# Kernel tuning notes

Hardware: AMD Instinct MI355X
Metric: run time of the kernel (lower is better)

The kernel has to match this reference:

```python
import jax, jax.numpy as jnp
import numpy as np

N, R, B, OUT, STD = 512, 4, 65536, 512, 0.01


def setup_inputs() -> dict:
    key = jax.random.key(0)
    ks = jax.random.split(key, 6)
    return {
        "x": jax.random.normal(ks[0], (B, N), jnp.float32),
        "G": jax.random.normal(ks[1], (N, R), jnp.float32) * STD,
        "H": jax.random.normal(ks[2], (N, R), jnp.float32) * STD,
        "b1": jax.random.normal(ks[3], (N,), jnp.float32) * STD,
        "W2": jax.random.normal(ks[4], (N, OUT), jnp.float32) * STD,
        "b2": jax.random.normal(ks[5], (OUT,), jnp.float32) * STD,
    }


def _shift_A(v):
    # Z_1 v: circular shift down with corner +1 (Toeplitz-like operator A)
    return jnp.concatenate([v[-1:], v[:-1]], axis=0)


def _shift_BT(v):
    # Z_{-1}^T v: shift up with corner -1 (Toeplitz-like operator B^T)
    return jnp.concatenate([v[1:], -v[:1]], axis=0)


def _krylov(shift_fn, V):
    # K[j, :, i] = A^j v_i, shape (n, n, r)
    def step(v, _):
        return shift_fn(v), v
    _, K = jax.lax.scan(step, V, None, length=V.shape[0])
    return K


def krylov_recon(G, H):
    # W = sum_i Krylov(Z_1, g_i) @ Krylov(Z_{-1}^T, h_i)^T, shape (n, n)
    KA = _krylov(_shift_A, G)   # (n, n, r)
    KB = _krylov(_shift_BT, H)  # (n, n, r)
    return jnp.einsum('jai,jbi->ab', KA, KB)


def reference(x, G, H, b1, W2, b2):
    W = krylov_recon(G, H)                 # (n, n) structured matrix
    h = jax.nn.relu(x @ W + b1)            # (B, n)
    return h @ W2 + b2                     # (B, out)
```

## Files before the change

kernel.cpp:

```cpp
#include <hip/hip_runtime.h>
#include <hip/hip_bf16.h>
#include <stdint.h>


typedef __attribute__((ext_vector_type(8))) short bf16x8;
typedef __attribute__((ext_vector_type(4))) float f32x4;
typedef __attribute__((ext_vector_type(4))) unsigned int u32x4;

__device__ __forceinline__ unsigned short f2bf(float f) {
  return __builtin_bit_cast(unsigned short, __float2bfloat16(f));
}

__global__ void build_w_partials(const float* __restrict__ G, const float* __restrict__ H,
                                 float* __restrict__ Wp) {
  __shared__ float4 Gs[512];
  __shared__ float4 Hs[512];
  const int t = threadIdx.x;
  const float4* G4 = (const float4*)G;
  const float4* H4 = (const float4*)H;
  for (int i = t; i < 512; i += 256) { Gs[i] = G4[i]; Hs[i] = H4[i]; }
  __syncthreads();

  const int blk  = blockIdx.x;
  const int tile = blk >> 2;
  const int jc   = blk & 3;
  const int a0 = (tile >> 3) << 6;
  const int b0 = (tile & 7) << 6;
  const int ab = a0 + ((t >> 4) << 2);
  const int bb = b0 + ((t & 15) << 2);

  float acc[4][4] = {};
  const int j0 = jc << 7;
  for (int jj = 0; jj < 128; ++jj) {
    const int j = j0 + jj;
    float4 Ga[4], Hb[4];
#pragma unroll
    for (int r = 0; r < 4; ++r) Ga[r] = Gs[(ab + r - j) & 511];
#pragma unroll
    for (int c = 0; c < 4; ++c) {
      const int idx = bb + c + j;
      const float s = (idx >= 512) ? -1.f : 1.f;
      const float4 hv = Hs[idx & 511];
      Hb[c].x = hv.x * s; Hb[c].y = hv.y * s; Hb[c].z = hv.z * s; Hb[c].w = hv.w * s;
    }
#pragma unroll
    for (int r = 0; r < 4; ++r)
#pragma unroll
      for (int c = 0; c < 4; ++c)
        acc[r][c] += Ga[r].x * Hb[c].x + Ga[r].y * Hb[c].y +
                     Ga[r].z * Hb[c].z + Ga[r].w * Hb[c].w;
  }

  float* outp = Wp + (size_t)jc * 262144;
#pragma unroll
  for (int r = 0; r < 4; ++r)
#pragma unroll
    for (int c = 0; c < 4; ++c)
      outp[(size_t)(ab + r) * 512 + (bb + c)] = acc[r][c];
}

__global__ void reduce_transpose_w(const float* __restrict__ Wp, unsigned short* __restrict__ Wt) {
  const int idx = blockIdx.x * 256 + threadIdx.x;
  const int b = idx >> 9, a = idx & 511;
  const size_t o = (size_t)a * 512 + b;
  float s = Wp[o] + Wp[o + 262144] + Wp[o + 524288] + Wp[o + 786432];
  Wt[(size_t)b * 512 + a] = f2bf(s);
}

__global__ void transpose_convert_w2(const float* __restrict__ W2, unsigned short* __restrict__ W2t) {
  const int idx = blockIdx.x * 256 + threadIdx.x;
  const int n = idx >> 9, k = idx & 511;
  W2t[(size_t)n * 512 + k] = f2bf(W2[(size_t)k * 512 + n]);
}

template <bool AF32>
__global__ __launch_bounds__(512, 2) void gemm_ring(
    const void* __restrict__ Ap, const unsigned short* __restrict__ Bt,
    const float* __restrict__ bias, void* __restrict__ Cp) {
  constexpr int NT    = 16;
  constexpr int RING  = AF32 ? 3 : 4;
  constexpr int ASLOT = AF32 ? 32768 : 16384;
  constexpr int BSLOT = 16384;
  constexpr int SLOT  = ASLOT + BSLOT;
  constexpr int NAG   = AF32 ? 4 : 2;
  constexpr int GPT   = NAG + 2;

  __shared__ __attribute__((aligned(16))) char lds[RING * SLOT];

  const int tid  = threadIdx.x;
  const int lane = tid & 63;
  const int w    = tid >> 6;
  const int wm   = w & 1;
  const int wn   = w >> 1;
  const int lr   = lane & 15;
  const int lq   = lane >> 4;

  const int bid = (int)blockIdx.x;
  const int wg  = (bid & 7) * 64 + (bid >> 3);
  const int m0  = (wg >> 1) << 8;
  const int n0  = (wg & 1) << 8;

  float bv[4];
#pragma unroll
  for (int ni = 0; ni < 4; ++ni) bv[ni] = bias[n0 + wn * 64 + ni * 16 + lr];
  asm volatile("s_waitcnt vmcnt(0) lgkmcnt(0)" ::: "memory");

  size_t aSrcOff[NAG];
  if constexpr (AF32) {
#pragma unroll
    for (int i = 0; i < 4; ++i) {
      const int cl = i * 512 + tid;
      const int r = cl >> 3, d = cl & 7;
      aSrcOff[i] = (size_t)r * 2048 + (size_t)((d ^ (r & 7)) << 4);
    }
  } else {
#pragma unroll
    for (int i = 0; i < 2; ++i) {
      const int cl = i * 512 + tid;
      const int r = cl >> 2, d = cl & 3;
      aSrcOff[i] = (size_t)r * 1024 + (size_t)((d ^ ((r >> 1) & 3)) << 4);
    }
  }
  size_t bSrcOff[2];
#pragma unroll
  for (int i = 0; i < 2; ++i) {
    const int cl = i * 512 + tid;
    const int r = cl >> 2, d = cl & 3;
    bSrcOff[i] = (size_t)r * 1024 + (size_t)((d ^ ((r >> 1) & 3)) << 4);
  }
  const char* aBase = (const char*)Ap + (size_t)m0 * (AF32 ? 2048 : 1024);
  const char* bBase = (const char*)Bt + (size_t)n0 * 1024;

  auto stage = [&](int kt) {
    char* sb = lds + (kt % RING) * SLOT;
#pragma unroll
    for (int i = 0; i < NAG; ++i)
      __builtin_amdgcn_global_load_lds(
        (const __attribute__((address_space(1))) void*)
          (aBase + aSrcOff[i] + (size_t)kt * (AF32 ? 128 : 64)),
        (__attribute__((address_space(3))) void*)(sb + i * 8192 + w * 1024),
        16, 0, 0);
#pragma unroll
    for (int i = 0; i < 2; ++i)
      __builtin_amdgcn_global_load_lds(
        (const __attribute__((address_space(1))) void*)
          (bBase + bSrcOff[i] + (size_t)kt * 64),
        (__attribute__((address_space(3))) void*)(sb + ASLOT + i * 8192 + w * 1024),
        16, 0, 0);
  };

  int offA[8], offB[4];
#pragma unroll
  for (int mi = 0; mi < 8; ++mi) {
    const int r = wm * 128 + mi * 16 + lr;
    if constexpr (AF32)
      offA[mi] = r * 128 + (((2 * lq) ^ (r & 7)) << 4);
    else
      offA[mi] = r * 64 + ((lq ^ ((r >> 1) & 3)) << 4);
  }
#pragma unroll
  for (int ni = 0; ni < 4; ++ni) {
    const int rb = wn * 64 + ni * 16 + lr;
    offB[ni] = ASLOT + rb * 64 + ((lq ^ ((rb >> 1) & 3)) << 4);
  }

  f32x4 acc[8][4];
  const f32x4 vz = {0.f, 0.f, 0.f, 0.f};
#pragma unroll
  for (int i = 0; i < 8; ++i)
#pragma unroll
    for (int j = 0; j < 4; ++j) acc[i][j] = vz;

#pragma unroll
  for (int p = 0; p < RING - 1; ++p) stage(p);
  if constexpr (AF32) asm volatile("s_waitcnt vmcnt(6)" ::: "memory");
  else                asm volatile("s_waitcnt vmcnt(8)" ::: "memory");
  __builtin_amdgcn_s_barrier();
  __builtin_amdgcn_sched_barrier(0);

#pragma unroll
  for (int t = 0; t < NT; ++t) {
    if (t + RING - 1 < NT) stage(t + RING - 1);

    const char* sb = lds + (t % RING) * SLOT;

    bf16x8 bfr[4];
#pragma unroll
    for (int ni = 0; ni < 4; ++ni) bfr[ni] = *(const bf16x8*)(sb + offB[ni]);

    if constexpr (AF32) {
      f32x4 lo[2][2], hi[2][2];
      bf16x8 afr[2];
#pragma unroll
      for (int p = 0; p < 2; ++p) {
        lo[0][p] = *(const f32x4*)(sb + offA[p]);
        hi[0][p] = *(const f32x4*)(sb + (offA[p] ^ 16));
      }
#pragma unroll
      for (int g = 0; g < 4; ++g) {
        if (g < 3) {
#pragma unroll
          for (int p = 0; p < 2; ++p) {
            lo[(g + 1) & 1][p] = *(const f32x4*)(sb + offA[2 * (g + 1) + p]);
            hi[(g + 1) & 1][p] = *(const f32x4*)(sb + (offA[2 * (g + 1) + p] ^ 16));
          }
        }
#pragma unroll
        for (int p = 0; p < 2; ++p) {
          const f32x4 l = lo[g & 1][p], h2 = hi[g & 1][p];
          unsigned int w0, w1, w2, w3;
          asm("v_cvt_pk_bf16_f32 %0, %1, %2" : "=v"(w0) : "v"(l.x), "v"(l.y));
          asm("v_cvt_pk_bf16_f32 %0, %1, %2" : "=v"(w1) : "v"(l.z), "v"(l.w));
          asm("v_cvt_pk_bf16_f32 %0, %1, %2" : "=v"(w2) : "v"(h2.x), "v"(h2.y));
          asm("v_cvt_pk_bf16_f32 %0, %1, %2" : "=v"(w3) : "v"(h2.z), "v"(h2.w));
          u32x4 pw = {w0, w1, w2, w3};
          afr[p] = __builtin_bit_cast(bf16x8, pw);
        }
        __builtin_amdgcn_s_setprio(1);
#pragma unroll
        for (int p = 0; p < 2; ++p)
#pragma unroll
          for (int ni = 0; ni < 4; ++ni)
            acc[2 * g + p][ni] =
                __builtin_amdgcn_mfma_f32_16x16x32_bf16(afr[p], bfr[ni], acc[2 * g + p][ni], 0, 0, 0);
        __builtin_amdgcn_s_setprio(0);
      }
    } else {
      bf16x8 afr[8];
#pragma unroll
      for (int p = 0; p < 2; ++p) afr[p] = *(const bf16x8*)(sb + offA[p]);
#pragma unroll
      for (int g = 0; g < 4; ++g) {
        if (g < 3) {
#pragma unroll
          for (int p = 0; p < 2; ++p)
            afr[2 * (g + 1) + p] = *(const bf16x8*)(sb + offA[2 * (g + 1) + p]);
        }
        __builtin_amdgcn_s_setprio(1);
#pragma unroll
        for (int p = 0; p < 2; ++p)
#pragma unroll
          for (int ni = 0; ni < 4; ++ni)
            acc[2 * g + p][ni] =
                __builtin_amdgcn_mfma_f32_16x16x32_bf16(afr[2 * g + p], bfr[ni], acc[2 * g + p][ni], 0, 0, 0);
        __builtin_amdgcn_s_setprio(0);
      }
    }

    if (t < NT - 1) {
      const int rem  = NT - 2 - t;
      const int keep = (rem < RING - 2 ? rem : RING - 2) * GPT;
      if (keep == 8)      asm volatile("s_waitcnt vmcnt(8)" ::: "memory");
      else if (keep == 6) asm volatile("s_waitcnt vmcnt(6)" ::: "memory");
      else if (keep == 4) asm volatile("s_waitcnt vmcnt(4)" ::: "memory");
      else                asm volatile("s_waitcnt vmcnt(0)" ::: "memory");
    }
    __builtin_amdgcn_s_barrier();
    __builtin_amdgcn_sched_barrier(0);
  }

#pragma unroll
  for (int ni = 0; ni < 4; ++ni) {
    const int gc = n0 + wn * 64 + ni * 16 + lr;
#pragma unroll
    for (int mi = 0; mi < 8; ++mi) {
      const int gr = m0 + wm * 128 + mi * 16 + lq * 4;
      const f32x4 v = acc[mi][ni];
#pragma unroll
      for (int i = 0; i < 4; ++i) {
        const float val = v[i] + bv[ni];
        if constexpr (AF32)
          ((unsigned short*)Cp)[(size_t)(gr + i) * 512 + gc] = f2bf(val > 0.f ? val : 0.f);
        else
          ((float*)Cp)[(size_t)(gr + i) * 512 + gc] = val;
      }
    }
  }
}

extern "C" void kernel_launch(void* const* d_in, const int* in_sizes, int n_in,
                              void* d_out, int out_size, void* d_ws, size_t ws_size,
                              hipStream_t stream) {
  (void)in_sizes; (void)n_in; (void)out_size; (void)ws_size;
  const float* x  = (const float*)d_in[0];
  const float* G  = (const float*)d_in[1];
  const float* H  = (const float*)d_in[2];
  const float* b1 = (const float*)d_in[3];
  const float* W2 = (const float*)d_in[4];
  const float* b2 = (const float*)d_in[5];
  float* out = (float*)d_out;

  char* ws = (char*)d_ws;
  unsigned short* h   = (unsigned short*)ws;
  unsigned short* Wt  = (unsigned short*)(ws + 67108864);
  unsigned short* W2t = (unsigned short*)(ws + 67633152);
  float*          Wp  = (float*)(ws + 68157440);

  build_w_partials<<<256, 256, 0, stream>>>(G, H, Wp);
  reduce_transpose_w<<<1024, 256, 0, stream>>>(Wp, Wt);
  transpose_convert_w2<<<1024, 256, 0, stream>>>(W2, W2t);
  gemm_ring<true><<<512, 512, 0, stream>>>((const void*)x, Wt, b1, (void*)h);
  gemm_ring<false><<<512, 512, 0, stream>>>((const void*)h, W2t, b2, (void*)out);
}
```

Baseline: 171.9 us.

## Shrink GEMM tiles to 128x128 with double-buffered LDS and more workgroups

Replaces the 256x256-tile, 512-thread GEMM that used a 3-4 deep async LDS ring with a 128x128-tile, 256-thread kernel using plain double buffering and __syncthreads. It launches 2048 workgroups instead of 512, targets 3 workgroups per CU, and drops the s_setprio and fine-grained vmcnt waits. The aim is higher occupancy and better load balance across CUs. The cost is lower arithmetic intensity per tile, so each operand is re-read from global memory more often, and less prefetch depth is available to hide latency.

```diff
diff --git a/kernel.cpp b/kernel.cpp
--- a/kernel.cpp
+++ b/kernel.cpp
@@ -74,18 +74,16 @@
 }
 
 template <bool AF32>
-__global__ __launch_bounds__(512, 2) void gemm_ring(
+__global__ __launch_bounds__(256, 3) void gemm_m97(
     const void* __restrict__ Ap, const unsigned short* __restrict__ Bt,
     const float* __restrict__ bias, void* __restrict__ Cp) {
   constexpr int NT    = 16;
-  constexpr int RING  = AF32 ? 3 : 4;
-  constexpr int ASLOT = AF32 ? 32768 : 16384;
-  constexpr int BSLOT = 16384;
-  constexpr int SLOT  = ASLOT + BSLOT;
+  constexpr int ASLOT = AF32 ? 16384 : 8192;
+  constexpr int BSLOT = 8192;
+  constexpr int BUF   = ASLOT + BSLOT;
   constexpr int NAG   = AF32 ? 4 : 2;
-  constexpr int GPT   = NAG + 2;
-
-  __shared__ __attribute__((aligned(16))) char lds[RING * SLOT];
+
+  __shared__ __attribute__((aligned(16))) char lds[2 * BUF];
 
   const int tid  = threadIdx.x;
   const int lane = tid & 63;
@@ -96,27 +94,26 @@
   const int lq   = lane >> 4;
 
   const int bid = (int)blockIdx.x;
-  const int wg  = (bid & 7) * 64 + (bid >> 3);
-  const int m0  = (wg >> 1) << 8;
-  const int n0  = (wg & 1) << 8;
+  const int wg  = (bid & 7) * 256 + (bid >> 3);
+  const int m0  = (wg >> 2) << 7;
+  const int n0  = (wg & 3) << 7;
 
   float bv[4];
 #pragma unroll
   for (int ni = 0; ni < 4; ++ni) bv[ni] = bias[n0 + wn * 64 + ni * 16 + lr];
-  asm volatile("s_waitcnt vmcnt(0) lgkmcnt(0)" ::: "memory");
 
   size_t aSrcOff[NAG];
   if constexpr (AF32) {
 #pragma unroll
     for (int i = 0; i < 4; ++i) {
-      const int cl = i * 512 + tid;
+      const int cl = i * 256 + tid;
       const int r = cl >> 3, d = cl & 7;
       aSrcOff[i] = (size_t)r * 2048 + (size_t)((d ^ (r & 7)) << 4);
     }
   } else {
 #pragma unroll
     for (int i = 0; i < 2; ++i) {
-      const int cl = i * 512 + tid;
+      const int cl = i * 256 + tid;
       const int r = cl >> 2, d = cl & 3;
       aSrcOff[i] = (size_t)r * 1024 + (size_t)((d ^ ((r >> 1) & 3)) << 4);
     }
@@ -124,35 +121,35 @@
   size_t bSrcOff[2];
 #pragma unroll
   for (int i = 0; i < 2; ++i) {
-    const int cl = i * 512 + tid;
+    const int cl = i * 256 + tid;
     const int r = cl >> 2, d = cl & 3;
     bSrcOff[i] = (size_t)r * 1024 + (size_t)((d ^ ((r >> 1) & 3)) << 4);
   }
   const char* aBase = (const char*)Ap + (size_t)m0 * (AF32 ? 2048 : 1024);
   const char* bBase = (const char*)Bt + (size_t)n0 * 1024;
 
-  auto stage = [&](int kt) {
-    char* sb = lds + (kt % RING) * SLOT;
+  auto stage = [&](int kt, int buf) {
+    char* sb = lds + buf * BUF;
 #pragma unroll
     for (int i = 0; i < NAG; ++i)
       __builtin_amdgcn_global_load_lds(
         (const __attribute__((address_space(1))) void*)
           (aBase + aSrcOff[i] + (size_t)kt * (AF32 ? 128 : 64)),
-        (__attribute__((address_space(3))) void*)(sb + i * 8192 + w * 1024),
+        (__attribute__((address_space(3))) void*)(sb + i * 4096 + w * 1024),
         16, 0, 0);
 #pragma unroll
     for (int i = 0; i < 2; ++i)
       __builtin_amdgcn_global_load_lds(
         (const __attribute__((address_space(1))) void*)
           (bBase + bSrcOff[i] + (size_t)kt * 64),
-        (__attribute__((address_space(3))) void*)(sb + ASLOT + i * 8192 + w * 1024),
+        (__attribute__((address_space(3))) void*)(sb + ASLOT + i * 4096 + w * 1024),
         16, 0, 0);
   };
 
-  int offA[8], offB[4];
-#pragma unroll
-  for (int mi = 0; mi < 8; ++mi) {
-    const int r = wm * 128 + mi * 16 + lr;
+  int offA[4], offB[4];
+#pragma unroll
+  for (int mi = 0; mi < 4; ++mi) {
+    const int r = wm * 64 + mi * 16 + lr;
     if constexpr (AF32)
       offA[mi] = r * 128 + (((2 * lq) ^ (r & 7)) << 4);
     else
@@ -164,107 +161,73 @@
     offB[ni] = ASLOT + rb * 64 + ((lq ^ ((rb >> 1) & 3)) << 4);
   }
 
-  f32x4 acc[8][4];
+  f32x4 acc[4][4];
   const f32x4 vz = {0.f, 0.f, 0.f, 0.f};
 #pragma unroll
-  for (int i = 0; i < 8; ++i)
+  for (int i = 0; i < 4; ++i)
 #pragma unroll
     for (int j = 0; j < 4; ++j) acc[i][j] = vz;
 
-#pragma unroll
-  for (int p = 0; p < RING - 1; ++p) stage(p);
-  if constexpr (AF32) asm volatile("s_waitcnt vmcnt(6)" ::: "memory");
-  else                asm volatile("s_waitcnt vmcnt(8)" ::: "memory");
-  __builtin_amdgcn_s_barrier();
-  __builtin_amdgcn_sched_barrier(0);
+  stage(0, 0);
+  __syncthreads();
 
 #pragma unroll
   for (int t = 0; t < NT; ++t) {
-    if (t + RING - 1 < NT) stage(t + RING - 1);
-
-    const char* sb = lds + (t % RING) * SLOT;
-
+    const int cur = t & 1;
+    if (t < NT - 1) stage(t + 1, cur ^ 1);
+
+    const char* sb = lds + cur * BUF;
     bf16x8 bfr[4];
 #pragma unroll
     for (int ni = 0; ni < 4; ++ni) bfr[ni] = *(const bf16x8*)(sb + offB[ni]);
 
     if constexpr (AF32) {
-      f32x4 lo[2][2], hi[2][2];
-      bf16x8 afr[2];
-#pragma unroll
-      for (int p = 0; p < 2; ++p) {
-        lo[0][p] = *(const f32x4*)(sb + offA[p]);
-        hi[0][p] = *(const f32x4*)(sb + (offA[p] ^ 16));
-      }
-#pragma unroll
-      for (int g = 0; g < 4; ++g) {
-        if (g < 3) {
-#pragma unroll
-          for (int p = 0; p < 2; ++p) {
-            lo[(g + 1) & 1][p] = *(const f32x4*)(sb + offA[2 * (g + 1) + p]);
-            hi[(g + 1) & 1][p] = *(const f32x4*)(sb + (offA[2 * (g + 1) + p] ^ 16));
-          }
+#pragma unroll
+      for (int g = 0; g < 2; ++g) {
+        f32x4 lo[2], hi[2];
+        bf16x8 afr[2];
+#pragma unroll
+        for (int p = 0; p < 2; ++p) {
+          lo[p] = *(const f32x4*)(sb + offA[2 * g + p]);
+          hi[p] = *(const f32x4*)(sb + (offA[2 * g + p] ^ 16));
         }
 #pragma unroll
         for (int p = 0; p < 2; ++p) {
-          const f32x4 l = lo[g & 1][p], h2 = hi[g & 1][p];
           unsigned int w0, w1, w2, w3;
-          asm("v_cvt_pk_bf16_f32 %0, %1, %2" : "=v"(w0) : "v"(l.x), "v"(l.y));
-          asm("v_cvt_pk_bf16_f32 %0, %1, %2" : "=v"(w1) : "v"(l.z), "v"(l.w));
-          asm("v_cvt_pk_bf16_f32 %0, %1, %2" : "=v"(w2) : "v"(h2.x), "v"(h2.y));
-          asm("v_cvt_pk_bf16_f32 %0, %1, %2" : "=v"(w3) : "v"(h2.z), "v"(h2.w));
+          asm("v_cvt_pk_bf16_f32 %0, %1, %2" : "=v"(w0) : "v"(lo[p].x), "v"(lo[p].y));
+          asm("v_cvt_pk_bf16_f32 %0, %1, %2" : "=v"(w1) : "v"(lo[p].z), "v"(lo[p].w));
+          asm("v_cvt_pk_bf16_f32 %0, %1, %2" : "=v"(w2) : "v"(hi[p].x), "v"(hi[p].y));
+          asm("v_cvt_pk_bf16_f32 %0, %1, %2" : "=v"(w3) : "v"(hi[p].z), "v"(hi[p].w));
           u32x4 pw = {w0, w1, w2, w3};
           afr[p] = __builtin_bit_cast(bf16x8, pw);
         }
-        __builtin_amdgcn_s_setprio(1);
 #pragma unroll
         for (int p = 0; p < 2; ++p)
 #pragma unroll
           for (int ni = 0; ni < 4; ++ni)
             acc[2 * g + p][ni] =
                 __builtin_amdgcn_mfma_f32_16x16x32_bf16(afr[p], bfr[ni], acc[2 * g + p][ni], 0, 0, 0);
-        __builtin_amdgcn_s_setprio(0);
       }
     } else {
-      bf16x8 afr[8];
-#pragma unroll
-      for (int p = 0; p < 2; ++p) afr[p] = *(const bf16x8*)(sb + offA[p]);
-#pragma unroll
-      for (int g = 0; g < 4; ++g) {
-        if (g < 3) {
-#pragma unroll
-          for (int p = 0; p < 2; ++p)
-            afr[2 * (g + 1) + p] = *(const bf16x8*)(sb + offA[2 * (g + 1) + p]);
-        }
-        __builtin_amdgcn_s_setprio(1);
-#pragma unroll
-        for (int p = 0; p < 2; ++p)
-#pragma unroll
-          for (int ni = 0; ni < 4; ++ni)
-            acc[2 * g + p][ni] =
-                __builtin_amdgcn_mfma_f32_16x16x32_bf16(afr[2 * g + p], bfr[ni], acc[2 * g + p][ni], 0, 0, 0);
-        __builtin_amdgcn_s_setprio(0);
-      }
-    }
-
-    if (t < NT - 1) {
-      const int rem  = NT - 2 - t;
-      const int keep = (rem < RING - 2 ? rem : RING - 2) * GPT;
-      if (keep == 8)      asm volatile("s_waitcnt vmcnt(8)" ::: "memory");
-      else if (keep == 6) asm volatile("s_waitcnt vmcnt(6)" ::: "memory");
-      else if (keep == 4) asm volatile("s_waitcnt vmcnt(4)" ::: "memory");
-      else                asm volatile("s_waitcnt vmcnt(0)" ::: "memory");
-    }
-    __builtin_amdgcn_s_barrier();
-    __builtin_amdgcn_sched_barrier(0);
+      bf16x8 afr[4];
+#pragma unroll
+      for (int mi = 0; mi < 4; ++mi) afr[mi] = *(const bf16x8*)(sb + offA[mi]);
+#pragma unroll
+      for (int mi = 0; mi < 4; ++mi)
+#pragma unroll
+        for (int ni = 0; ni < 4; ++ni)
+          acc[mi][ni] = __builtin_amdgcn_mfma_f32_16x16x32_bf16(afr[mi], bfr[ni], acc[mi][ni], 0, 0, 0);
+    }
+
+    __syncthreads();
   }
 
 #pragma unroll
   for (int ni = 0; ni < 4; ++ni) {
     const int gc = n0 + wn * 64 + ni * 16 + lr;
 #pragma unroll
-    for (int mi = 0; mi < 8; ++mi) {
-      const int gr = m0 + wm * 128 + mi * 16 + lq * 4;
+    for (int mi = 0; mi < 4; ++mi) {
+      const int gr = m0 + wm * 64 + mi * 16 + lq * 4;
       const f32x4 v = acc[mi][ni];
 #pragma unroll
       for (int i = 0; i < 4; ++i) {
@@ -299,6 +262,6 @@
   build_w_partials<<<256, 256, 0, stream>>>(G, H, Wp);
   reduce_transpose_w<<<1024, 256, 0, stream>>>(Wp, Wt);
   transpose_convert_w2<<<1024, 256, 0, stream>>>(W2, W2t);
-  gemm_ring<true><<<512, 512, 0, stream>>>((const void*)x, Wt, b1, (void*)h);
-  gemm_ring<false><<<512, 512, 0, stream>>>((const void*)h, W2t, b2, (void*)out);
-}
+  gemm_m97<true><<<2048, 256, 0, stream>>>((const void*)x, Wt, b1, (void*)h);
+  gemm_m97<false><<<2048, 256, 0, stream>>>((const void*)h, W2t, b2, (void*)out);
+}
```

Result: slower. 185.3 us (+7.8%).
